# Performance work log

Measured on AMD Instinct MI355X. Metric: run time of the kernel, lower is better.

## Reference

```python
import jax, jax.numpy as jnp
import numpy as np

# Plain-RNN variant of RNNX (output_sizes=None): 2 stacked Elman layers,
# per layer: h' = tanh(Linear(concat(x, h))). batch_first=False -> Xt is [T, B, I].
T, B, I, H = 512, 128, 256, 512


def setup_inputs() -> dict:
    key = jax.random.key(0)
    k0, k1, k2, k3, k4 = jax.random.split(key, 5)
    stdv = 1.0 / np.sqrt(H)  # reset_parameters: uniform(-1/sqrt(hs), 1/sqrt(hs))
    return {
        "Xt": jax.random.normal(k0, (T, B, I), dtype=jnp.float32),
        "W1": jax.random.uniform(k1, (I + H, H), dtype=jnp.float32, minval=-stdv, maxval=stdv),
        "b1": jax.random.uniform(k2, (H,), dtype=jnp.float32, minval=-stdv, maxval=stdv),
        "W2": jax.random.uniform(k3, (H + H, H), dtype=jnp.float32, minval=-stdv, maxval=stdv),
        "b2": jax.random.uniform(k4, (H,), dtype=jnp.float32, minval=-stdv, maxval=stdv),
    }


def reference(Xt, W1, b1, W2, b2):
    # Xt: [T, B, I]; returns (out [T, B, H] stacked layer-2 outputs, hidden [2, B, H])
    Bsz = Xt.shape[1]
    Hd = W1.shape[1]
    h0 = (jnp.zeros((Bsz, Hd), Xt.dtype), jnp.zeros((Bsz, Hd), Xt.dtype))

    def step(h, x_t):
        h1, h2 = h
        y1 = jnp.tanh(jnp.concatenate([x_t, h1], axis=-1) @ W1 + b1)  # layer 1
        y2 = jnp.tanh(jnp.concatenate([y1, h2], axis=-1) @ W2 + b2)   # layer 2
        return (y1, y2), y2

    (h1f, h2f), out = jax.lax.scan(step, h0, Xt)
    hidden = jnp.stack([h1f, h2f], axis=0)  # [n_layers, B, H]
    return out, hidden
```

## Files before the change

kernel.cpp:

```cpp
#include <hip/hip_runtime.h>
#include <hip/hip_bf16.h>

#define TT 512
#define BB 128
#define II 256
#define HH 512

#define NGROUP 8
#define WPG    16
#define NWG    (NGROUP * WPG)

typedef __attribute__((ext_vector_type(8))) unsigned short ushort8;
typedef __attribute__((ext_vector_type(8))) __bf16        bf16x8;
typedef __attribute__((ext_vector_type(4))) float         float4v;

union frag8 { ushort8 u; bf16x8 b; };

__device__ __forceinline__ unsigned short f2bf(float f) {
    union { float f; unsigned u; } v; v.f = f;
    unsigned r = (v.u + 0x7FFFu + ((v.u >> 16) & 1u)) >> 16;
    return (unsigned short)r;
}
__device__ __forceinline__ float bf2f(unsigned short h) {
    union { unsigned u; float f; } v; v.u = ((unsigned)h) << 16;
    return v.f;
}
__device__ __forceinline__ float tanh_fast(float x) {
    float e = __expf(2.0f * x);
    return 1.0f - 2.0f / (e + 1.0f);
}
__device__ __forceinline__ float4v mfma(bf16x8 a, bf16x8 b, float4v c) {
    return __builtin_amdgcn_mfma_f32_16x16x32_bf16(a, b, c, 0, 0, 0);
}

__global__ __launch_bounds__(256, 1) void rnn_fused(
    const float* __restrict__ Xt,
    const float* __restrict__ W1,
    const float* __restrict__ b1,
    const float* __restrict__ W2,
    const float* __restrict__ b2,
    float* __restrict__ out,
    unsigned short* __restrict__ Ybuf,
    unsigned int* __restrict__ cnt)
{
    const int wg  = blockIdx.x;
    const int g   = wg & 7;
    const int j   = wg >> 3;
    const int tid = threadIdx.x;
    const int w   = tid >> 6;
    const int c   = w & 1;
    const int kh  = w >> 1;
    const int l   = tid & 63;
    const int lr  = l & 15;
    const int lq  = l >> 4;
    const int n0  = j * 32 + c * 16;
    const int row0 = g * 16;

    unsigned short* Y1 = Ybuf;
    unsigned short* Y2 = Ybuf + 2 * BB * HH;

    __shared__ float lds[2][2][64][4];

    frag8 w1h[12], w1l[12], w2h[16], w2l[16];
    const int kb1 = kh * 12, kb2 = kh * 16;
#pragma unroll
    for (int q = 0; q < 12; ++q) {
#pragma unroll
        for (int e = 0; e < 8; ++e) {
            float v = W1[((kb1 + q) * 32 + lq * 8 + e) * HH + n0 + lr];
            unsigned short hi = f2bf(v);
            w1h[q].u[e] = hi;
            w1l[q].u[e] = f2bf(v - bf2f(hi));
        }
    }
#pragma unroll
    for (int q = 0; q < 16; ++q) {
#pragma unroll
        for (int e = 0; e < 8; ++e) {
            float v = W2[((kb2 + q) * 32 + lq * 8 + e) * HH + n0 + lr];
            unsigned short hi = f2bf(v);
            w2h[q].u[e] = hi;
            w2l[q].u[e] = f2bf(v - bf2f(hi));
        }
    }
    const float bias1 = (kh == 0) ? b1[n0 + lr] : 0.0f;
    const float bias2 = (kh == 0) ? b2[n0 + lr] : 0.0f;

#pragma unroll 1
    for (int t = 0; t <= TT; ++t) {
        const int par = t & 1;
        const unsigned short* y1r = Y1 + (par ^ 1) * (BB * HH);
        const unsigned short* y2r = Y2 + par * (BB * HH);

        frag8 a1[16];
#pragma unroll
        for (int q = 0; q < 16; ++q)
            a1[q].u = *(const ushort8*)(y1r + (row0 + lr) * HH + q * 32 + lq * 8);

        float4v acc1 = {bias1, bias1, bias1, bias1};
        float4v acc2 = {bias2, bias2, bias2, bias2};

        if (kh == 0) {
            if (t < TT) {
#pragma unroll
                for (int q = 0; q < 8; ++q) {
                    const float* xp = Xt + ((size_t)t * BB + row0 + lr) * II + q * 32 + lq * 8;
                    frag8 ax;
#pragma unroll
                    for (int e = 0; e < 8; ++e) ax.u[e] = f2bf(xp[e]);
                    acc1 = mfma(ax.b, w1h[q].b, acc1);
                    acc1 = mfma(ax.b, w1l[q].b, acc1);
                }
#pragma unroll
                for (int q = 0; q < 4; ++q) {
                    acc1 = mfma(a1[q].b, w1h[8 + q].b, acc1);
                    acc1 = mfma(a1[q].b, w1l[8 + q].b, acc1);
                }
            }
            if (t >= 1) {
#pragma unroll
                for (int q = 0; q < 16; ++q) {
                    acc2 = mfma(a1[q].b, w2h[q].b, acc2);
                    acc2 = mfma(a1[q].b, w2l[q].b, acc2);
                }
            }
        } else {
            if (t < TT) {
#pragma unroll
                for (int q = 0; q < 12; ++q) {
                    acc1 = mfma(a1[4 + q].b, w1h[q].b, acc1);
                    acc1 = mfma(a1[4 + q].b, w1l[q].b, acc1);
                }
            }
            if (t >= 1) {
                frag8 a2[16];
#pragma unroll
                for (int q = 0; q < 16; ++q)
                    a2[q].u = *(const ushort8*)(y2r + (row0 + lr) * HH + q * 32 + lq * 8);
#pragma unroll
                for (int q = 0; q < 16; ++q) {
                    acc2 = mfma(a2[q].b, w2h[q].b, acc2);
                    acc2 = mfma(a2[q].b, w2l[q].b, acc2);
                }
            }
            *(float4v*)&lds[0][c][l][0] = acc1;
            *(float4v*)&lds[1][c][l][0] = acc2;
        }
        __syncthreads();

        if (kh == 0) {
            float4v p1 = *(const float4v*)&lds[0][c][l][0];
            float4v p2 = *(const float4v*)&lds[1][c][l][0];
            if (t < TT) {
                unsigned short* y1w = Y1 + par * (BB * HH);
#pragma unroll
                for (int i = 0; i < 4; ++i) {
                    float y = tanh_fast(acc1[i] + p1[i]);
                    int r = row0 + lq * 4 + i;
                    y1w[r * HH + n0 + lr] = f2bf(y);
                    if (t == TT - 1)
                        out[(size_t)TT * BB * HH + (size_t)r * HH + n0 + lr] = y;
                }
            }
            if (t >= 1) {
                unsigned short* y2w = Y2 + (par ^ 1) * (BB * HH);
#pragma unroll
                for (int i = 0; i < 4; ++i) {
                    float y = tanh_fast(acc2[i] + p2[i]);
                    int r = row0 + lq * 4 + i;
                    y2w[r * HH + n0 + lr] = f2bf(y);
                    out[((size_t)(t - 1) * BB + r) * HH + n0 + lr] = y;
                    if (t == TT)
                        out[(size_t)TT * BB * HH + (size_t)BB * HH + (size_t)r * HH + n0 + lr] = y;
                }
            }
        }

        if (t < TT) {
            __syncthreads();
            if (tid == 0) {
                unsigned int* cp = cnt + g * 1024 + t;
                __hip_atomic_fetch_add(cp, 1u, __ATOMIC_RELEASE, __HIP_MEMORY_SCOPE_AGENT);
                while (__hip_atomic_load(cp, __ATOMIC_RELAXED, __HIP_MEMORY_SCOPE_AGENT) < WPG)
                    __builtin_amdgcn_s_sleep(2);
                __builtin_amdgcn_fence(__ATOMIC_ACQUIRE, "agent");
            }
            __syncthreads();
        }
    }
}

extern "C" void kernel_launch(void* const* d_in, const int* in_sizes, int n_in,
                              void* d_out, int out_size, void* d_ws, size_t ws_size,
                              hipStream_t stream) {
    const float* Xt = (const float*)d_in[0];
    const float* W1 = (const float*)d_in[1];
    const float* b1 = (const float*)d_in[2];
    const float* W2 = (const float*)d_in[3];
    const float* b2 = (const float*)d_in[4];
    float* out = (float*)d_out;

    unsigned short* Ybuf = (unsigned short*)d_ws;
    unsigned int*   cnt  = (unsigned int*)((char*)d_ws + 4 * BB * HH * 2);
    size_t zero_bytes = (size_t)4 * BB * HH * 2 + (size_t)NGROUP * 1024 * 4;

    hipMemsetAsync(d_ws, 0, zero_bytes, stream);
    hipLaunchKernelGGL(rnn_fused, dim3(NWG), dim3(256), 0, stream,
                       Xt, W1, b1, W2, b2, out, Ybuf, cnt);
}
```

Baseline: 4.863 ms.

## Rebalance reduction epilogue, use relaxed atomic Y traffic and overlap output stores with barrier

Splits each accumulator into two independent chains so consecutive MFMAs no longer serialize on one accumulator. The epilogue is rebalanced: wave half kh=0 finishes layer 1 and kh=1 finishes layer 2, each reading the other half's partial sum from LDS. Results are transposed through LDS so the Y state is written as 8-byte agent-scope atomic stores, and Y is read back with relaxed atomic loads. The release/acquire fences are replaced by an explicit waitcnt plus relaxed counter updates, and the fp32 output stores are moved after the arrive so they overlap the spin-wait. The relaxed memory ordering depends on the explicit waitcnt and the atomic loads bypassing stale caches, which is a correctness risk.

New measurement: 5.468 ms. 1.12x slower.

```diff
diff --git a/kernel.cpp b/kernel.cpp
--- a/kernel.cpp
+++ b/kernel.cpp
@@ -11,15 +11,15 @@
 #define NWG    (NGROUP * WPG)
 
 typedef __attribute__((ext_vector_type(8))) unsigned short ushort8;
-typedef __attribute__((ext_vector_type(8))) __bf16        bf16x8;
-typedef __attribute__((ext_vector_type(4))) float         float4v;
-
-union frag8 { ushort8 u; bf16x8 b; };
+typedef __attribute__((ext_vector_type(8))) __bf16         bf16x8;
+typedef __attribute__((ext_vector_type(4))) float          float4v;
+typedef unsigned long long u64;
+
+union frag8 { ushort8 u; bf16x8 b; u64 q[2]; };
 
 __device__ __forceinline__ unsigned short f2bf(float f) {
     union { float f; unsigned u; } v; v.f = f;
-    unsigned r = (v.u + 0x7FFFu + ((v.u >> 16) & 1u)) >> 16;
-    return (unsigned short)r;
+    return (unsigned short)((v.u + 0x7FFFu + ((v.u >> 16) & 1u)) >> 16);
 }
 __device__ __forceinline__ float bf2f(unsigned short h) {
     union { unsigned u; float f; } v; v.u = ((unsigned)h) << 16;
@@ -31,6 +31,12 @@
 }
 __device__ __forceinline__ float4v mfma(bf16x8 a, bf16x8 b, float4v c) {
     return __builtin_amdgcn_mfma_f32_16x16x32_bf16(a, b, c, 0, 0, 0);
+}
+__device__ __forceinline__ u64 ald(const unsigned short* p) {
+    return __hip_atomic_load((u64*)(void*)p, __ATOMIC_RELAXED, __HIP_MEMORY_SCOPE_AGENT);
+}
+__device__ __forceinline__ void ast(unsigned short* p, u64 v) {
+    __hip_atomic_store((u64*)(void*)p, v, __ATOMIC_RELAXED, __HIP_MEMORY_SCOPE_AGENT);
 }
 
 __global__ __launch_bounds__(256, 1) void rnn_fused(
@@ -59,12 +65,14 @@
     unsigned short* Y1 = Ybuf;
     unsigned short* Y2 = Ybuf + 2 * BB * HH;
 
-    __shared__ float lds[2][2][64][4];
+    __shared__ float lp1[2][64][4];
+    __shared__ float lp2[2][64][4];
+    __shared__ __align__(8) unsigned short tr[4][16][20];
 
     frag8 w1h[12], w1l[12], w2h[16], w2l[16];
     const int kb1 = kh * 12, kb2 = kh * 16;
 #pragma unroll
-    for (int q = 0; q < 12; ++q) {
+    for (int q = 0; q < 12; ++q)
 #pragma unroll
         for (int e = 0; e < 8; ++e) {
             float v = W1[((kb1 + q) * 32 + lq * 8 + e) * HH + n0 + lr];
@@ -72,9 +80,8 @@
             w1h[q].u[e] = hi;
             w1l[q].u[e] = f2bf(v - bf2f(hi));
         }
-    }
-#pragma unroll
-    for (int q = 0; q < 16; ++q) {
+#pragma unroll
+    for (int q = 0; q < 16; ++q)
 #pragma unroll
         for (int e = 0; e < 8; ++e) {
             float v = W2[((kb2 + q) * 32 + lq * 8 + e) * HH + n0 + lr];
@@ -82,108 +89,155 @@
             w2h[q].u[e] = hi;
             w2l[q].u[e] = f2bf(v - bf2f(hi));
         }
-    }
-    const float bias1 = (kh == 0) ? b1[n0 + lr] : 0.0f;
-    const float bias2 = (kh == 0) ? b2[n0 + lr] : 0.0f;
+    const float bias1 = b1[n0 + lr];
+    const float bias2 = b2[n0 + lr];
 
 #pragma unroll 1
     for (int t = 0; t <= TT; ++t) {
         const int par = t & 1;
         const unsigned short* y1r = Y1 + (par ^ 1) * (BB * HH);
         const unsigned short* y2r = Y2 + par * (BB * HH);
-
-        frag8 a1[16];
-#pragma unroll
-        for (int q = 0; q < 16; ++q)
-            a1[q].u = *(const ushort8*)(y1r + (row0 + lr) * HH + q * 32 + lq * 8);
-
-        float4v acc1 = {bias1, bias1, bias1, bias1};
-        float4v acc2 = {bias2, bias2, bias2, bias2};
+        unsigned short* y1w = Y1 + par * (BB * HH);
+        unsigned short* y2w = Y2 + (par ^ 1) * (BB * HH);
+
+        frag8 a1[16], a2[16];
+        if (kh == 0) {
+#pragma unroll
+            for (int q = 0; q < 16; ++q) {
+                const unsigned short* p = y1r + (row0 + lr) * HH + q * 32 + lq * 8;
+                a1[q].q[0] = ald(p); a1[q].q[1] = ald(p + 4);
+            }
+        } else {
+#pragma unroll
+            for (int q = 4; q < 16; ++q) {
+                const unsigned short* p = y1r + (row0 + lr) * HH + q * 32 + lq * 8;
+                a1[q].q[0] = ald(p); a1[q].q[1] = ald(p + 4);
+            }
+            if (t >= 1) {
+#pragma unroll
+                for (int q = 0; q < 16; ++q) {
+                    const unsigned short* p = y2r + (row0 + lr) * HH + q * 32 + lq * 8;
+                    a2[q].q[0] = ald(p); a2[q].q[1] = ald(p + 4);
+                }
+            }
+        }
+
+        float4v acc1  = {bias1, bias1, bias1, bias1};
+        float4v acc1b = {0.f, 0.f, 0.f, 0.f};
+        float4v acc2  = {bias2, bias2, bias2, bias2};
+        float4v acc2b = {0.f, 0.f, 0.f, 0.f};
+        if (kh == 0) acc2 = acc1b;
+        else         acc1 = acc1b;
 
         if (kh == 0) {
             if (t < TT) {
 #pragma unroll
                 for (int q = 0; q < 8; ++q) {
                     const float* xp = Xt + ((size_t)t * BB + row0 + lr) * II + q * 32 + lq * 8;
+                    float4v x0 = *(const float4v*)xp;
+                    float4v x1 = *(const float4v*)(xp + 4);
                     frag8 ax;
 #pragma unroll
-                    for (int e = 0; e < 8; ++e) ax.u[e] = f2bf(xp[e]);
-                    acc1 = mfma(ax.b, w1h[q].b, acc1);
-                    acc1 = mfma(ax.b, w1l[q].b, acc1);
+                    for (int e = 0; e < 4; ++e) { ax.u[e] = f2bf(x0[e]); ax.u[4 + e] = f2bf(x1[e]); }
+                    acc1  = mfma(ax.b, w1h[q].b, acc1);
+                    acc1b = mfma(ax.b, w1l[q].b, acc1b);
                 }
 #pragma unroll
                 for (int q = 0; q < 4; ++q) {
-                    acc1 = mfma(a1[q].b, w1h[8 + q].b, acc1);
-                    acc1 = mfma(a1[q].b, w1l[8 + q].b, acc1);
+                    acc1  = mfma(a1[q].b, w1h[8 + q].b, acc1);
+                    acc1b = mfma(a1[q].b, w1l[8 + q].b, acc1b);
                 }
             }
             if (t >= 1) {
 #pragma unroll
                 for (int q = 0; q < 16; ++q) {
-                    acc2 = mfma(a1[q].b, w2h[q].b, acc2);
-                    acc2 = mfma(a1[q].b, w2l[q].b, acc2);
+                    acc2  = mfma(a1[q].b, w2h[q].b, acc2);
+                    acc2b = mfma(a1[q].b, w2l[q].b, acc2b);
                 }
             }
         } else {
             if (t < TT) {
 #pragma unroll
                 for (int q = 0; q < 12; ++q) {
-                    acc1 = mfma(a1[4 + q].b, w1h[q].b, acc1);
-                    acc1 = mfma(a1[4 + q].b, w1l[q].b, acc1);
+                    acc1  = mfma(a1[4 + q].b, w1h[q].b, acc1);
+                    acc1b = mfma(a1[4 + q].b, w1l[q].b, acc1b);
                 }
             }
             if (t >= 1) {
-                frag8 a2[16];
-#pragma unroll
-                for (int q = 0; q < 16; ++q)
-                    a2[q].u = *(const ushort8*)(y2r + (row0 + lr) * HH + q * 32 + lq * 8);
 #pragma unroll
                 for (int q = 0; q < 16; ++q) {
-                    acc2 = mfma(a2[q].b, w2h[q].b, acc2);
-                    acc2 = mfma(a2[q].b, w2l[q].b, acc2);
-                }
-            }
-            *(float4v*)&lds[0][c][l][0] = acc1;
-            *(float4v*)&lds[1][c][l][0] = acc2;
-        }
+                    acc2  = mfma(a2[q].b, w2h[q].b, acc2);
+                    acc2b = mfma(a2[q].b, w2l[q].b, acc2b);
+                }
+            }
+        }
+
+        if (kh == 1 && t < TT)  *(float4v*)&lp1[c][l][0] = acc1 + acc1b;
+        if (kh == 0 && t >= 1)  *(float4v*)&lp2[c][l][0] = acc2 + acc2b;
         __syncthreads();
 
-        if (kh == 0) {
-            float4v p1 = *(const float4v*)&lds[0][c][l][0];
-            float4v p2 = *(const float4v*)&lds[1][c][l][0];
-            if (t < TT) {
-                unsigned short* y1w = Y1 + par * (BB * HH);
-#pragma unroll
-                for (int i = 0; i < 4; ++i) {
-                    float y = tanh_fast(acc1[i] + p1[i]);
-                    int r = row0 + lq * 4 + i;
-                    y1w[r * HH + n0 + lr] = f2bf(y);
-                    if (t == TT - 1)
-                        out[(size_t)TT * BB * HH + (size_t)r * HH + n0 + lr] = y;
-                }
-            }
-            if (t >= 1) {
-                unsigned short* y2w = Y2 + (par ^ 1) * (BB * HH);
-#pragma unroll
-                for (int i = 0; i < 4; ++i) {
-                    float y = tanh_fast(acc2[i] + p2[i]);
-                    int r = row0 + lq * 4 + i;
-                    y2w[r * HH + n0 + lr] = f2bf(y);
-                    out[((size_t)(t - 1) * BB + r) * HH + n0 + lr] = y;
-                    if (t == TT)
-                        out[(size_t)TT * BB * HH + (size_t)BB * HH + (size_t)r * HH + n0 + lr] = y;
-                }
+        float yout[4];
+        if (kh == 0 && t < TT) {
+            float4v p = *(const float4v*)&lp1[c][l][0];
+#pragma unroll
+            for (int i = 0; i < 4; ++i) {
+                float y = tanh_fast(acc1[i] + acc1b[i] + p[i]);
+                tr[w][lq * 4 + i][lr] = f2bf(y);
+                yout[i] = y;
+            }
+        }
+        if (kh == 1 && t >= 1) {
+            float4v p = *(const float4v*)&lp2[c][l][0];
+#pragma unroll
+            for (int i = 0; i < 4; ++i) {
+                float y = tanh_fast(acc2[i] + acc2b[i] + p[i]);
+                tr[w][lq * 4 + i][lr] = f2bf(y);
+                yout[i] = y;
+            }
+        }
+        {
+            const int row = l & 15, ch = l >> 4;
+            if (kh == 0 && t < TT) {
+                u64 v = *(const u64*)&tr[w][row][ch * 4];
+                ast(y1w + (row0 + row) * HH + n0 + ch * 4, v);
+            }
+            if (kh == 1 && t >= 1) {
+                u64 v = *(const u64*)&tr[w][row][ch * 4];
+                ast(y2w + (row0 + row) * HH + n0 + ch * 4, v);
+            }
+        }
+
+        asm volatile("s_waitcnt vmcnt(0) lgkmcnt(0)" ::: "memory");
+        __syncthreads();
+
+        if (t < TT && tid == 0)
+            __hip_atomic_fetch_add(cnt + g * 1024 + t, 1u, __ATOMIC_RELAXED,
+                                   __HIP_MEMORY_SCOPE_AGENT);
+
+        if (kh == 1 && t >= 1) {
+#pragma unroll
+            for (int i = 0; i < 4; ++i) {
+                const int r = row0 + lq * 4 + i;
+                __builtin_nontemporal_store(yout[i], &out[((size_t)(t - 1) * BB + r) * HH + n0 + lr]);
+                if (t == TT)
+                    __builtin_nontemporal_store(yout[i],
+                        &out[(size_t)TT * BB * HH + (size_t)BB * HH + (size_t)r * HH + n0 + lr]);
+            }
+        }
+        if (kh == 0 && t == TT - 1) {
+#pragma unroll
+            for (int i = 0; i < 4; ++i) {
+                const int r = row0 + lq * 4 + i;
+                __builtin_nontemporal_store(yout[i],
+                    &out[(size_t)TT * BB * HH + (size_t)r * HH + n0 + lr]);
             }
         }
 
         if (t < TT) {
-            __syncthreads();
             if (tid == 0) {
-                unsigned int* cp = cnt + g * 1024 + t;
-                __hip_atomic_fetch_add(cp, 1u, __ATOMIC_RELEASE, __HIP_MEMORY_SCOPE_AGENT);
-                while (__hip_atomic_load(cp, __ATOMIC_RELAXED, __HIP_MEMORY_SCOPE_AGENT) < WPG)
-                    __builtin_amdgcn_s_sleep(2);
-                __builtin_amdgcn_fence(__ATOMIC_ACQUIRE, "agent");
+                while (__hip_atomic_load(cnt + g * 1024 + t, __ATOMIC_RELAXED,
+                                         __HIP_MEMORY_SCOPE_AGENT) < WPG)
+                    __builtin_amdgcn_s_sleep(1);
             }
             __syncthreads();
         }
```
